# Performance work log

Hardware: AMD Instinct MI355X
Metric: run time of the kernel (lower is better)

## Reference

```python
import jax, jax.numpy as jnp
import numpy as np

N_NODES = 10000
N_EDGES = 320000
IN_DIM = 128
HID = 256


def setup_inputs() -> dict:
    key = jax.random.key(0)
    ks = jax.random.split(key, 10)
    s_in = 1.0 / np.sqrt(IN_DIM)
    s_h = 1.0 / np.sqrt(HID)
    return {
        "x": jax.random.normal(ks[0], (N_NODES, IN_DIM), dtype=jnp.float32),
        "edge_index": jax.random.randint(ks[1], (2, N_EDGES), 0, N_NODES, dtype=jnp.int64),
        # feature_projector Linear(IN_DIM -> HID)
        "Wp": jax.random.uniform(ks[2], (IN_DIM, HID), jnp.float32, -s_in, s_in),
        "bp": jax.random.uniform(ks[3], (HID,), jnp.float32, -s_in, s_in),
        # LSTM(input=HID, hidden=HID) params, torch layout [4H, H], gate order i,f,g,o
        "W_ih": jax.random.uniform(ks[4], (4 * HID, HID), jnp.float32, -s_h, s_h),
        "W_hh": jax.random.uniform(ks[5], (4 * HID, HID), jnp.float32, -s_h, s_h),
        "b_ih": jax.random.uniform(ks[6], (4 * HID,), jnp.float32, -s_h, s_h),
        "b_hh": jax.random.uniform(ks[7], (4 * HID,), jnp.float32, -s_h, s_h),
        # EvolveGCN-O initial weight [H, H] (glorot-style)
        "initial_weight": jax.random.normal(ks[8], (HID, HID), dtype=jnp.float32) * np.sqrt(2.0 / (2 * HID)),
        # GCNConv bias
        "b_gcn": jnp.zeros((HID,), dtype=jnp.float32),
    }


def _forward(x, edge_index, Wp, bp, W_ih, W_hh, b_ih, b_hh, initial_weight, b_gcn):
    n = x.shape[0]
    # 1) feature projection
    h = x @ Wp + bp  # [N, H]
    # 2) EvolveGCN-O: one LSTM step on the weight matrix (rows = batch),
    #    with h0 = c0 = initial_weight; evolved hidden state is the GCN weight.
    gates = initial_weight @ W_ih.T + b_ih + initial_weight @ W_hh.T + b_hh  # [H, 4H]
    i_g, f_g, g_g, o_g = jnp.split(gates, 4, axis=-1)
    c = jax.nn.sigmoid(f_g) * initial_weight + jax.nn.sigmoid(i_g) * jnp.tanh(g_g)
    W = jax.nn.sigmoid(o_g) * jnp.tanh(c)  # [H, H]
    # 3) GCN propagation with fixed W: out = D^{-1/2}(A+I)D^{-1/2} (h W) + b
    hw = h @ W  # [N, H]
    self_loop = jnp.arange(n, dtype=edge_index.dtype)
    src = jnp.concatenate([edge_index[0], self_loop])
    dst = jnp.concatenate([edge_index[1], self_loop])
    ones = jnp.ones(src.shape[0], dtype=hw.dtype)
    deg = jax.ops.segment_sum(ones, dst, num_segments=n)  # in-degree incl. self loop
    dinv = jnp.where(deg > 0, jax.lax.rsqrt(deg), 0.0)
    norm = dinv[src] * dinv[dst]  # [E+N]
    out = jax.ops.segment_sum(hw[src] * norm[:, None], dst, num_segments=n)
    return out + b_gcn


def reference(x, edge_index, Wp, bp, W_ih, W_hh, b_ih, b_hh, initial_weight, b_gcn):
    return _forward(x, edge_index, Wp, bp, W_ih, W_hh, b_ih, b_hh, initial_weight, b_gcn)
```

## Files before the change

kernel.cpp:

```cpp
#include <hip/hip_runtime.h>
#include <math.h>

#define N_NODES 10000
#define N_EDGES 320000
#define IN_DIM  128
#define HID     256
#define CAP     128
#define NWB     64
#define NFB     448
#define NXB     128
#define NB1     (NWB + NFB + NXB)

typedef __attribute__((ext_vector_type(8))) short frag_ab;
typedef __attribute__((ext_vector_type(4))) float frag_cd;


__device__ __forceinline__ unsigned bf16rne(float f) {
    union { float f; unsigned u; } c; c.f = f;
    return (c.u + 0x7FFFu + ((c.u >> 16) & 1u)) >> 16;
}
__device__ __forceinline__ float sig_f(float x)  { return 1.f / (1.f + __expf(-x)); }
__device__ __forceinline__ float tanh_f(float x) { return 1.f - 2.f / (1.f + __expf(2.f * x)); }

__global__ __launch_bounds__(256, 2)
void k1_prep(const float* __restrict__ x, const int* __restrict__ ei,
             const float* __restrict__ Wp, const float* __restrict__ bp,
             const float* __restrict__ wih, const float* __restrict__ whh,
             const float* __restrict__ b_ih, const float* __restrict__ b_hh,
             const float* __restrict__ iw,
             int* __restrict__ cursor, unsigned* __restrict__ wct,
             float* __restrict__ bc, unsigned* __restrict__ xb,
             int* __restrict__ bucket) {
    __shared__ __align__(16) char smem_raw[57920];
    const int bid = blockIdx.x;
    const int t = threadIdx.x;

    if (bid < NWB) {
        float (*aT)[260]  = (float(*)[260])smem_raw;
        float (*bSt)[20]  = (float(*)[20])(smem_raw + 33280);
        float (*iwc)[260] = (float(*)[260])(smem_raw + 53760);
        #pragma unroll
        for (int n = 0; n < 16; ++n) {
            int nrow = (n >> 2) * 256 + 4 * bid + (n & 3);
            bSt[t][n] = wih[nrow * 256 + t] + whh[nrow * 256 + t];
        }
        const int mg = t >> 2, ng = t & 3;
        const int srow = t >> 3, sf4 = t & 7;
        float acc[4][4] = {};
        for (int kt = 0; kt < 8; ++kt) {
            int k0 = kt * 32;
            __syncthreads();
            #pragma unroll
            for (int rr = 0; rr < 8; ++rr) {
                int row = srow + 32 * rr;
                float4 v = *(const float4*)&iw[row * 256 + k0 + 4 * sf4];
                aT[4 * sf4 + 0][row] = v.x; aT[4 * sf4 + 1][row] = v.y;
                aT[4 * sf4 + 2][row] = v.z; aT[4 * sf4 + 3][row] = v.w;
            }
            __syncthreads();
            if (kt == (bid >> 3)) {
                int c0 = (4 * bid) & 31;
                #pragma unroll
                for (int jj = 0; jj < 4; ++jj) iwc[jj][t] = aT[c0 + jj][t];
            }
            #pragma unroll 4
            for (int kk = 0; kk < 32; ++kk) {
                float4 a4 = *(const float4*)&aT[kk][4 * mg];
                float4 b4 = *(const float4*)&bSt[k0 + kk][4 * ng];
                float a[4] = {a4.x, a4.y, a4.z, a4.w};
                float b[4] = {b4.x, b4.y, b4.z, b4.w};
                #pragma unroll
                for (int i = 0; i < 4; ++i)
                    #pragma unroll
                    for (int j = 0; j < 4; ++j)
                        acc[i][j] = fmaf(a[i], b[j], acc[i][j]);
            }
        }
        float (*gates_lds)[17] = (float(*)[17])smem_raw;
        float (*wevc)[260]     = (float(*)[260])(smem_raw + 33280);
        __syncthreads();
        #pragma unroll
        for (int i = 0; i < 4; ++i)
            #pragma unroll
            for (int j = 0; j < 4; ++j)
                gates_lds[4 * mg + i][4 * ng + j] = acc[i][j];
        __syncthreads();
        {
            int r = t;
            #pragma unroll
            for (int jj = 0; jj < 4; ++jj) {
                int jcol = 4 * bid + jj;
                float gi = gates_lds[r][0  + jj] + b_ih[jcol]       + b_hh[jcol];
                float gf = gates_lds[r][4  + jj] + b_ih[256 + jcol] + b_hh[256 + jcol];
                float gg = gates_lds[r][8  + jj] + b_ih[512 + jcol] + b_hh[512 + jcol];
                float go = gates_lds[r][12 + jj] + b_ih[768 + jcol] + b_hh[768 + jcol];
                float c  = sig_f(gf) * iwc[jj][r] + sig_f(gi) * tanh_f(gg);
                wevc[jj][r] = sig_f(go) * tanh_f(c);
            }
        }
        float (*wpT)[132] = (float(*)[132])smem_raw;
        const int a2 = t & 63, jj = t >> 6;
        float c0 = 0.f, c1 = 0.f;
        for (int kt2 = 0; kt2 < 8; ++kt2) {
            int k0 = kt2 * 32;
            __syncthreads();
            #pragma unroll
            for (int ri = 0; ri < 4; ++ri) {
                int a = srow + 32 * ri;
                float4 v = *(const float4*)&Wp[a * 256 + k0 + 4 * sf4];
                wpT[4 * sf4 + 0][a] = v.x; wpT[4 * sf4 + 1][a] = v.y;
                wpT[4 * sf4 + 2][a] = v.z; wpT[4 * sf4 + 3][a] = v.w;
            }
            __syncthreads();
            #pragma unroll 8
            for (int kk = 0; kk < 32; ++kk) {
                float2 wv = *(const float2*)&wpT[kk][2 * a2];
                float wev = wevc[jj][k0 + kk];
                c0 = fmaf(wv.x, wev, c0);
                c1 = fmaf(wv.y, wev, c1);
            }
        }
        wct[(4 * bid + jj) * 64 + a2] = bf16rne(c0) | (bf16rne(c1) << 16);
        if (t < 4) {
            float s = 0.f;
            #pragma unroll 4
            for (int k4 = 0; k4 < 64; ++k4) {
                float4 b4 = *(const float4*)&bp[4 * k4];
                float4 w4 = *(const float4*)&wevc[t][4 * k4];
                s = fmaf(b4.x, w4.x, fmaf(b4.y, w4.y, fmaf(b4.z, w4.z, fmaf(b4.w, w4.w, s))));
            }
            bc[4 * bid + t] = s;
        }
    } else if (bid < NWB + NFB) {
        for (int u = (bid - NWB) * 256 + t; u < N_EDGES / 4; u += NFB * 256) {
            int4 s4 = *(const int4*)&ei[u * 4];
            int4 d4 = *(const int4*)&ei[N_EDGES + u * 4];
            int p0 = atomicAdd(&cursor[d4.x], 1);
            if (p0 < CAP) bucket[d4.x * CAP + p0] = s4.x;
            int p1 = atomicAdd(&cursor[d4.y], 1);
            if (p1 < CAP) bucket[d4.y * CAP + p1] = s4.y;
            int p2 = atomicAdd(&cursor[d4.z], 1);
            if (p2 < CAP) bucket[d4.z * CAP + p2] = s4.z;
            int p3 = atomicAdd(&cursor[d4.w], 1);
            if (p3 < CAP) bucket[d4.w * CAP + p3] = s4.w;
        }
    } else {
        const float4* x4 = (const float4*)x;
        uint2* xb2 = (uint2*)xb;
        for (int idx = (bid - NWB - NFB) * 256 + t; idx < N_NODES * 32; idx += NXB * 256) {
            float4 v = x4[idx];
            xb2[idx] = make_uint2(bf16rne(v.x) | (bf16rne(v.y) << 16),
                                  bf16rne(v.z) | (bf16rne(v.w) << 16));
        }
    }
}

__global__ __launch_bounds__(256)
void k2_agg_out(const unsigned* __restrict__ xb, const int* __restrict__ cursor,
                const int* __restrict__ bucket, const unsigned* __restrict__ wct,
                const float* __restrict__ bc, const float* __restrict__ b_gcn,
                float* __restrict__ out) {
    __shared__ unsigned y_lds[16][64];
    __shared__ float rs_lds[16];
    const int t = threadIdx.x;
    const int tile = blockIdx.x;
    const int w = t >> 6, lane = t & 63;
    const int q = lane >> 4, ln = lane & 15;

    for (int vi = 0; vi < 4; ++vi) {
        int r = vi * 4 + w;
        int v = tile * 16 + r;
        int cntv = cursor[v];
        float dv = rsqrtf((float)(cntv + 1));
        int cnt2 = cntv > CAP ? CAP : cntv;
        unsigned self = xb[v * 64 + lane];
        union { unsigned u; float f; } c0, c1;
        c0.u = self << 16; c1.u = self & 0xFFFF0000u;
        float acc0 = dv * c0.f, acc1 = dv * c1.f, wsum = dv;
        const int4* bkt4 = (const int4*)&bucket[v * CAP];
        int j = 0;
        for (; j + 8 <= cnt2; j += 8) {
            int4 sa = bkt4[j >> 2];
            int4 sb = bkt4[(j >> 2) + 1];
            float w0 = rsqrtf((float)(cursor[sa.x] + 1));
            float w1 = rsqrtf((float)(cursor[sa.y] + 1));
            float w2 = rsqrtf((float)(cursor[sa.z] + 1));
            float w3 = rsqrtf((float)(cursor[sa.w] + 1));
            float w4 = rsqrtf((float)(cursor[sb.x] + 1));
            float w5 = rsqrtf((float)(cursor[sb.y] + 1));
            float w6 = rsqrtf((float)(cursor[sb.z] + 1));
            float w7 = rsqrtf((float)(cursor[sb.w] + 1));
            unsigned r0 = xb[sa.x * 64 + lane];
            unsigned r1 = xb[sa.y * 64 + lane];
            unsigned r2 = xb[sa.z * 64 + lane];
            unsigned r3 = xb[sa.w * 64 + lane];
            unsigned r4 = xb[sb.x * 64 + lane];
            unsigned r5 = xb[sb.y * 64 + lane];
            unsigned r6 = xb[sb.z * 64 + lane];
            unsigned r7 = xb[sb.w * 64 + lane];
            union { unsigned u; float f; } a0, a1;
            a0.u = r0 << 16; a1.u = r0 & 0xFFFF0000u;
            acc0 = fmaf(w0, a0.f, acc0); acc1 = fmaf(w0, a1.f, acc1);
            a0.u = r1 << 16; a1.u = r1 & 0xFFFF0000u;
            acc0 = fmaf(w1, a0.f, acc0); acc1 = fmaf(w1, a1.f, acc1);
            a0.u = r2 << 16; a1.u = r2 & 0xFFFF0000u;
            acc0 = fmaf(w2, a0.f, acc0); acc1 = fmaf(w2, a1.f, acc1);
            a0.u = r3 << 16; a1.u = r3 & 0xFFFF0000u;
            acc0 = fmaf(w3, a0.f, acc0); acc1 = fmaf(w3, a1.f, acc1);
            a0.u = r4 << 16; a1.u = r4 & 0xFFFF0000u;
            acc0 = fmaf(w4, a0.f, acc0); acc1 = fmaf(w4, a1.f, acc1);
            a0.u = r5 << 16; a1.u = r5 & 0xFFFF0000u;
            acc0 = fmaf(w5, a0.f, acc0); acc1 = fmaf(w5, a1.f, acc1);
            a0.u = r6 << 16; a1.u = r6 & 0xFFFF0000u;
            acc0 = fmaf(w6, a0.f, acc0); acc1 = fmaf(w6, a1.f, acc1);
            a0.u = r7 << 16; a1.u = r7 & 0xFFFF0000u;
            acc0 = fmaf(w7, a0.f, acc0); acc1 = fmaf(w7, a1.f, acc1);
            wsum += w0 + w1 + w2 + w3 + w4 + w5 + w6 + w7;
        }
        for (; j < cnt2; ++j) {
            int s = bucket[v * CAP + j];
            float ws = rsqrtf((float)(cursor[s] + 1));
            unsigned rr = xb[s * 64 + lane];
            union { unsigned u; float f; } a0, a1;
            a0.u = rr << 16; a1.u = rr & 0xFFFF0000u;
            acc0 = fmaf(ws, a0.f, acc0); acc1 = fmaf(ws, a1.f, acc1);
            wsum += ws;
        }
        y_lds[r][lane] = bf16rne(dv * acc0) | (bf16rne(dv * acc1) << 16);
        if (lane == 0) rs_lds[r] = dv * wsum;
    }
    __syncthreads();

    const int4* ya   = (const int4*)&y_lds[0][0];
    const int4* wct4 = (const int4*)wct;
    union { int4 v; frag_ab f; } a[4];
    #pragma unroll
    for (int kc = 0; kc < 4; ++kc)
        a[kc].v = ya[ln * 16 + kc * 4 + q];
    float rsv[4];
    #pragma unroll
    for (int r = 0; r < 4; ++r) rsv[r] = rs_lds[q * 4 + r];
    #pragma unroll
    for (int i = 0; i < 4; ++i) {
        int n0 = (w + 4 * i) * 16;
        union { int4 v; frag_ab f; } b[4];
        #pragma unroll
        for (int kc = 0; kc < 4; ++kc)
            b[kc].v = wct4[(n0 + ln) * 16 + kc * 4 + q];
        frag_cd accd = {0.f, 0.f, 0.f, 0.f};
        #pragma unroll
        for (int kc = 0; kc < 4; ++kc)
            accd = __builtin_amdgcn_mfma_f32_16x16x32_bf16(a[kc].f, b[kc].f, accd, 0, 0, 0);
        int n = n0 + ln;
        float bcv = bc[n], bgv = b_gcn[n];
        #pragma unroll
        for (int r = 0; r < 4; ++r) {
            int m = tile * 16 + q * 4 + r;
            out[m * HID + n] = accd[r] + rsv[r] * bcv + bgv;
        }
    }
}

extern "C" void kernel_launch(void* const* d_in, const int* in_sizes, int n_in,
                              void* d_out, int out_size, void* d_ws, size_t ws_size,
                              hipStream_t stream) {
    const float* x     = (const float*)d_in[0];
    const int*   ei    = (const int*)d_in[1];
    const float* Wp    = (const float*)d_in[2];
    const float* bp    = (const float*)d_in[3];
    const float* W_ih  = (const float*)d_in[4];
    const float* W_hh  = (const float*)d_in[5];
    const float* b_ih  = (const float*)d_in[6];
    const float* b_hh  = (const float*)d_in[7];
    const float* iw    = (const float*)d_in[8];
    const float* b_gcn = (const float*)d_in[9];
    float* out = (float*)d_out;

    char* ws = (char*)d_ws;
    int*      cursor = (int*)     (ws + 0);
    unsigned* wct    = (unsigned*)(ws + 40064);
    float*    bc     = (float*)   (ws + 105600);
    unsigned* xb     = (unsigned*)(ws + 106624);
    int*      bucket = (int*)     (ws + 2666624);

    hipMemsetAsync(cursor, 0, N_NODES * sizeof(int), stream);

    k1_prep<<<NB1, 256, 0, stream>>>(x, ei, Wp, bp, W_ih, W_hh, b_ih, b_hh, iw,
                                     cursor, wct, bc, xb, bucket);
    k2_agg_out<<<625, 256, 0, stream>>>(xb, cursor, bucket, wct, bc, b_gcn, out);
}
```

Before: 150.4 us.

## Split fused prep and aggregate/output kernels into four separate kernels

Breaks the heterogeneous prep kernel into a weight-evolution kernel and a bucket/convert kernel, and splits aggregation from the MFMA output GEMM. Aggregation now uses one wave per node across 2500 blocks and writes the bf16 aggregate and row scale to a global workspace, which k_out reads back. This is meant to give the gather stage more parallelism and to stop the LSTM blocks from stalling the edge-bucketing blocks. In exchange it adds two kernel launches and a global round trip for the intermediate, and the weight kernel now runs alone with only 64 blocks, serialized before the bucketing kernel on the same stream.

```diff
diff --git a/kernel.cpp b/kernel.cpp
--- a/kernel.cpp
+++ b/kernel.cpp
@@ -7,9 +7,9 @@
 #define HID     256
 #define CAP     128
 #define NWB     64
+#define NXB     128
 #define NFB     448
-#define NXB     128
-#define NB1     (NWB + NFB + NXB)
+#define NBB     (NXB + NFB)
 
 typedef __attribute__((ext_vector_type(8))) short frag_ab;
 typedef __attribute__((ext_vector_type(4))) float frag_cd;
@@ -23,116 +23,128 @@
 __device__ __forceinline__ float tanh_f(float x) { return 1.f - 2.f / (1.f + __expf(2.f * x)); }
 
 __global__ __launch_bounds__(256, 2)
-void k1_prep(const float* __restrict__ x, const int* __restrict__ ei,
-             const float* __restrict__ Wp, const float* __restrict__ bp,
-             const float* __restrict__ wih, const float* __restrict__ whh,
-             const float* __restrict__ b_ih, const float* __restrict__ b_hh,
-             const float* __restrict__ iw,
-             int* __restrict__ cursor, unsigned* __restrict__ wct,
-             float* __restrict__ bc, unsigned* __restrict__ xb,
-             int* __restrict__ bucket) {
+void k_w(const float* __restrict__ Wp, const float* __restrict__ bp,
+         const float* __restrict__ wih, const float* __restrict__ whh,
+         const float* __restrict__ b_ih, const float* __restrict__ b_hh,
+         const float* __restrict__ iw,
+         unsigned* __restrict__ wct, float* __restrict__ bc) {
     __shared__ __align__(16) char smem_raw[57920];
     const int bid = blockIdx.x;
     const int t = threadIdx.x;
 
-    if (bid < NWB) {
-        float (*aT)[260]  = (float(*)[260])smem_raw;
-        float (*bSt)[20]  = (float(*)[20])(smem_raw + 33280);
-        float (*iwc)[260] = (float(*)[260])(smem_raw + 53760);
-        #pragma unroll
-        for (int n = 0; n < 16; ++n) {
-            int nrow = (n >> 2) * 256 + 4 * bid + (n & 3);
-            bSt[t][n] = wih[nrow * 256 + t] + whh[nrow * 256 + t];
-        }
-        const int mg = t >> 2, ng = t & 3;
-        const int srow = t >> 3, sf4 = t & 7;
-        float acc[4][4] = {};
-        for (int kt = 0; kt < 8; ++kt) {
-            int k0 = kt * 32;
-            __syncthreads();
+    float (*aT)[260]  = (float(*)[260])smem_raw;
+    float (*bSt)[20]  = (float(*)[20])(smem_raw + 33280);
+    float (*iwc)[260] = (float(*)[260])(smem_raw + 53760);
+    #pragma unroll
+    for (int n = 0; n < 16; ++n) {
+        int nrow = (n >> 2) * 256 + 4 * bid + (n & 3);
+        bSt[t][n] = wih[nrow * 256 + t] + whh[nrow * 256 + t];
+    }
+    const int mg = t >> 2, ng = t & 3;
+    const int srow = t >> 3, sf4 = t & 7;
+    float acc[4][4] = {};
+    for (int kt = 0; kt < 8; ++kt) {
+        int k0 = kt * 32;
+        __syncthreads();
+        #pragma unroll
+        for (int rr = 0; rr < 8; ++rr) {
+            int row = srow + 32 * rr;
+            float4 v = *(const float4*)&iw[row * 256 + k0 + 4 * sf4];
+            aT[4 * sf4 + 0][row] = v.x; aT[4 * sf4 + 1][row] = v.y;
+            aT[4 * sf4 + 2][row] = v.z; aT[4 * sf4 + 3][row] = v.w;
+        }
+        __syncthreads();
+        if (kt == (bid >> 3)) {
+            int c0 = (4 * bid) & 31;
             #pragma unroll
-            for (int rr = 0; rr < 8; ++rr) {
-                int row = srow + 32 * rr;
-                float4 v = *(const float4*)&iw[row * 256 + k0 + 4 * sf4];
-                aT[4 * sf4 + 0][row] = v.x; aT[4 * sf4 + 1][row] = v.y;
-                aT[4 * sf4 + 2][row] = v.z; aT[4 * sf4 + 3][row] = v.w;
-            }
-            __syncthreads();
-            if (kt == (bid >> 3)) {
-                int c0 = (4 * bid) & 31;
+            for (int jj = 0; jj < 4; ++jj) iwc[jj][t] = aT[c0 + jj][t];
+        }
+        #pragma unroll 4
+        for (int kk = 0; kk < 32; ++kk) {
+            float4 a4 = *(const float4*)&aT[kk][4 * mg];
+            float4 b4 = *(const float4*)&bSt[k0 + kk][4 * ng];
+            float a[4] = {a4.x, a4.y, a4.z, a4.w};
+            float b[4] = {b4.x, b4.y, b4.z, b4.w};
+            #pragma unroll
+            for (int i = 0; i < 4; ++i)
                 #pragma unroll
-                for (int jj = 0; jj < 4; ++jj) iwc[jj][t] = aT[c0 + jj][t];
-            }
-            #pragma unroll 4
-            for (int kk = 0; kk < 32; ++kk) {
-                float4 a4 = *(const float4*)&aT[kk][4 * mg];
-                float4 b4 = *(const float4*)&bSt[k0 + kk][4 * ng];
-                float a[4] = {a4.x, a4.y, a4.z, a4.w};
-                float b[4] = {b4.x, b4.y, b4.z, b4.w};
-                #pragma unroll
-                for (int i = 0; i < 4; ++i)
-                    #pragma unroll
-                    for (int j = 0; j < 4; ++j)
-                        acc[i][j] = fmaf(a[i], b[j], acc[i][j]);
-            }
-        }
-        float (*gates_lds)[17] = (float(*)[17])smem_raw;
-        float (*wevc)[260]     = (float(*)[260])(smem_raw + 33280);
-        __syncthreads();
-        #pragma unroll
-        for (int i = 0; i < 4; ++i)
-            #pragma unroll
-            for (int j = 0; j < 4; ++j)
-                gates_lds[4 * mg + i][4 * ng + j] = acc[i][j];
-        __syncthreads();
-        {
-            int r = t;
-            #pragma unroll
-            for (int jj = 0; jj < 4; ++jj) {
-                int jcol = 4 * bid + jj;
-                float gi = gates_lds[r][0  + jj] + b_ih[jcol]       + b_hh[jcol];
-                float gf = gates_lds[r][4  + jj] + b_ih[256 + jcol] + b_hh[256 + jcol];
-                float gg = gates_lds[r][8  + jj] + b_ih[512 + jcol] + b_hh[512 + jcol];
-                float go = gates_lds[r][12 + jj] + b_ih[768 + jcol] + b_hh[768 + jcol];
-                float c  = sig_f(gf) * iwc[jj][r] + sig_f(gi) * tanh_f(gg);
-                wevc[jj][r] = sig_f(go) * tanh_f(c);
-            }
-        }
-        float (*wpT)[132] = (float(*)[132])smem_raw;
-        const int a2 = t & 63, jj = t >> 6;
-        float c0 = 0.f, c1 = 0.f;
-        for (int kt2 = 0; kt2 < 8; ++kt2) {
-            int k0 = kt2 * 32;
-            __syncthreads();
-            #pragma unroll
-            for (int ri = 0; ri < 4; ++ri) {
-                int a = srow + 32 * ri;
-                float4 v = *(const float4*)&Wp[a * 256 + k0 + 4 * sf4];
-                wpT[4 * sf4 + 0][a] = v.x; wpT[4 * sf4 + 1][a] = v.y;
-                wpT[4 * sf4 + 2][a] = v.z; wpT[4 * sf4 + 3][a] = v.w;
-            }
-            __syncthreads();
-            #pragma unroll 8
-            for (int kk = 0; kk < 32; ++kk) {
-                float2 wv = *(const float2*)&wpT[kk][2 * a2];
-                float wev = wevc[jj][k0 + kk];
-                c0 = fmaf(wv.x, wev, c0);
-                c1 = fmaf(wv.y, wev, c1);
-            }
-        }
-        wct[(4 * bid + jj) * 64 + a2] = bf16rne(c0) | (bf16rne(c1) << 16);
-        if (t < 4) {
-            float s = 0.f;
-            #pragma unroll 4
-            for (int k4 = 0; k4 < 64; ++k4) {
-                float4 b4 = *(const float4*)&bp[4 * k4];
-                float4 w4 = *(const float4*)&wevc[t][4 * k4];
-                s = fmaf(b4.x, w4.x, fmaf(b4.y, w4.y, fmaf(b4.z, w4.z, fmaf(b4.w, w4.w, s))));
-            }
-            bc[4 * bid + t] = s;
-        }
-    } else if (bid < NWB + NFB) {
-        for (int u = (bid - NWB) * 256 + t; u < N_EDGES / 4; u += NFB * 256) {
+                for (int j = 0; j < 4; ++j)
+                    acc[i][j] = fmaf(a[i], b[j], acc[i][j]);
+        }
+    }
+    float (*gates_lds)[17] = (float(*)[17])smem_raw;
+    float (*wevc)[260]     = (float(*)[260])(smem_raw + 33280);
+    __syncthreads();
+    #pragma unroll
+    for (int i = 0; i < 4; ++i)
+        #pragma unroll
+        for (int j = 0; j < 4; ++j)
+            gates_lds[4 * mg + i][4 * ng + j] = acc[i][j];
+    __syncthreads();
+    {
+        int r = t;
+        #pragma unroll
+        for (int jj = 0; jj < 4; ++jj) {
+            int jcol = 4 * bid + jj;
+            float gi = gates_lds[r][0  + jj] + b_ih[jcol]       + b_hh[jcol];
+            float gf = gates_lds[r][4  + jj] + b_ih[256 + jcol] + b_hh[256 + jcol];
+            float gg = gates_lds[r][8  + jj] + b_ih[512 + jcol] + b_hh[512 + jcol];
+            float go = gates_lds[r][12 + jj] + b_ih[768 + jcol] + b_hh[768 + jcol];
+            float c  = sig_f(gf) * iwc[jj][r] + sig_f(gi) * tanh_f(gg);
+            wevc[jj][r] = sig_f(go) * tanh_f(c);
+        }
+    }
+    float (*wpT)[132] = (float(*)[132])smem_raw;
+    const int a2 = t & 63, jj = t >> 6;
+    float c0 = 0.f, c1 = 0.f;
+    for (int kt2 = 0; kt2 < 8; ++kt2) {
+        int k0 = kt2 * 32;
+        __syncthreads();
+        #pragma unroll
+        for (int ri = 0; ri < 4; ++ri) {
+            int a = srow + 32 * ri;
+            float4 v = *(const float4*)&Wp[a * 256 + k0 + 4 * sf4];
+            wpT[4 * sf4 + 0][a] = v.x; wpT[4 * sf4 + 1][a] = v.y;
+            wpT[4 * sf4 + 2][a] = v.z; wpT[4 * sf4 + 3][a] = v.w;
+        }
+        __syncthreads();
+        #pragma unroll 8
+        for (int kk = 0; kk < 32; ++kk) {
+            float2 wv = *(const float2*)&wpT[kk][2 * a2];
+            float wev = wevc[jj][k0 + kk];
+            c0 = fmaf(wv.x, wev, c0);
+            c1 = fmaf(wv.y, wev, c1);
+        }
+    }
+    wct[(4 * bid + jj) * 64 + a2] = bf16rne(c0) | (bf16rne(c1) << 16);
+    if (t < 4) {
+        float s = 0.f;
+        #pragma unroll 4
+        for (int k4 = 0; k4 < 64; ++k4) {
+            float4 b4 = *(const float4*)&bp[4 * k4];
+            float4 w4 = *(const float4*)&wevc[t][4 * k4];
+            s = fmaf(b4.x, w4.x, fmaf(b4.y, w4.y, fmaf(b4.z, w4.z, fmaf(b4.w, w4.w, s))));
+        }
+        bc[4 * bid + t] = s;
+    }
+}
+
+__global__ __launch_bounds__(256)
+void k_b(const float* __restrict__ x, const int* __restrict__ ei,
+         int* __restrict__ cursor, unsigned* __restrict__ xb,
+         int* __restrict__ bucket) {
+    const int bid = blockIdx.x;
+    const int t = threadIdx.x;
+    if (bid < NXB) {
+        const float4* x4 = (const float4*)x;
+        uint2* xb2 = (uint2*)xb;
+        for (int idx = bid * 256 + t; idx < N_NODES * 32; idx += NXB * 256) {
+            float4 v = x4[idx];
+            xb2[idx] = make_uint2(bf16rne(v.x) | (bf16rne(v.y) << 16),
+                                  bf16rne(v.z) | (bf16rne(v.w) << 16));
+        }
+    } else {
+        for (int u = (bid - NXB) * 256 + t; u < N_EDGES / 4; u += NFB * 256) {
             int4 s4 = *(const int4*)&ei[u * 4];
             int4 d4 = *(const int4*)&ei[N_EDGES + u * 4];
             int p0 = atomicAdd(&cursor[d4.x], 1);
@@ -144,102 +156,92 @@
             int p3 = atomicAdd(&cursor[d4.w], 1);
             if (p3 < CAP) bucket[d4.w * CAP + p3] = s4.w;
         }
-    } else {
-        const float4* x4 = (const float4*)x;
-        uint2* xb2 = (uint2*)xb;
-        for (int idx = (bid - NWB - NFB) * 256 + t; idx < N_NODES * 32; idx += NXB * 256) {
-            float4 v = x4[idx];
-            xb2[idx] = make_uint2(bf16rne(v.x) | (bf16rne(v.y) << 16),
-                                  bf16rne(v.z) | (bf16rne(v.w) << 16));
-        }
     }
 }
 
 __global__ __launch_bounds__(256)
-void k2_agg_out(const unsigned* __restrict__ xb, const int* __restrict__ cursor,
-                const int* __restrict__ bucket, const unsigned* __restrict__ wct,
-                const float* __restrict__ bc, const float* __restrict__ b_gcn,
-                float* __restrict__ out) {
-    __shared__ unsigned y_lds[16][64];
-    __shared__ float rs_lds[16];
+void k_agg(const unsigned* __restrict__ xb, const int* __restrict__ cursor,
+           const int* __restrict__ bucket, unsigned* __restrict__ yb,
+           float* __restrict__ rs) {
     const int t = threadIdx.x;
-    const int tile = blockIdx.x;
-    const int w = t >> 6, lane = t & 63;
-    const int q = lane >> 4, ln = lane & 15;
-
-    for (int vi = 0; vi < 4; ++vi) {
-        int r = vi * 4 + w;
-        int v = tile * 16 + r;
-        int cntv = cursor[v];
-        float dv = rsqrtf((float)(cntv + 1));
-        int cnt2 = cntv > CAP ? CAP : cntv;
-        unsigned self = xb[v * 64 + lane];
-        union { unsigned u; float f; } c0, c1;
-        c0.u = self << 16; c1.u = self & 0xFFFF0000u;
-        float acc0 = dv * c0.f, acc1 = dv * c1.f, wsum = dv;
-        const int4* bkt4 = (const int4*)&bucket[v * CAP];
-        int j = 0;
-        for (; j + 8 <= cnt2; j += 8) {
-            int4 sa = bkt4[j >> 2];
-            int4 sb = bkt4[(j >> 2) + 1];
-            float w0 = rsqrtf((float)(cursor[sa.x] + 1));
-            float w1 = rsqrtf((float)(cursor[sa.y] + 1));
-            float w2 = rsqrtf((float)(cursor[sa.z] + 1));
-            float w3 = rsqrtf((float)(cursor[sa.w] + 1));
-            float w4 = rsqrtf((float)(cursor[sb.x] + 1));
-            float w5 = rsqrtf((float)(cursor[sb.y] + 1));
-            float w6 = rsqrtf((float)(cursor[sb.z] + 1));
-            float w7 = rsqrtf((float)(cursor[sb.w] + 1));
-            unsigned r0 = xb[sa.x * 64 + lane];
-            unsigned r1 = xb[sa.y * 64 + lane];
-            unsigned r2 = xb[sa.z * 64 + lane];
-            unsigned r3 = xb[sa.w * 64 + lane];
-            unsigned r4 = xb[sb.x * 64 + lane];
-            unsigned r5 = xb[sb.y * 64 + lane];
-            unsigned r6 = xb[sb.z * 64 + lane];
-            unsigned r7 = xb[sb.w * 64 + lane];
-            union { unsigned u; float f; } a0, a1;
-            a0.u = r0 << 16; a1.u = r0 & 0xFFFF0000u;
-            acc0 = fmaf(w0, a0.f, acc0); acc1 = fmaf(w0, a1.f, acc1);
-            a0.u = r1 << 16; a1.u = r1 & 0xFFFF0000u;
-            acc0 = fmaf(w1, a0.f, acc0); acc1 = fmaf(w1, a1.f, acc1);
-            a0.u = r2 << 16; a1.u = r2 & 0xFFFF0000u;
-            acc0 = fmaf(w2, a0.f, acc0); acc1 = fmaf(w2, a1.f, acc1);
-            a0.u = r3 << 16; a1.u = r3 & 0xFFFF0000u;
-            acc0 = fmaf(w3, a0.f, acc0); acc1 = fmaf(w3, a1.f, acc1);
-            a0.u = r4 << 16; a1.u = r4 & 0xFFFF0000u;
-            acc0 = fmaf(w4, a0.f, acc0); acc1 = fmaf(w4, a1.f, acc1);
-            a0.u = r5 << 16; a1.u = r5 & 0xFFFF0000u;
-            acc0 = fmaf(w5, a0.f, acc0); acc1 = fmaf(w5, a1.f, acc1);
-            a0.u = r6 << 16; a1.u = r6 & 0xFFFF0000u;
-            acc0 = fmaf(w6, a0.f, acc0); acc1 = fmaf(w6, a1.f, acc1);
-            a0.u = r7 << 16; a1.u = r7 & 0xFFFF0000u;
-            acc0 = fmaf(w7, a0.f, acc0); acc1 = fmaf(w7, a1.f, acc1);
-            wsum += w0 + w1 + w2 + w3 + w4 + w5 + w6 + w7;
-        }
-        for (; j < cnt2; ++j) {
-            int s = bucket[v * CAP + j];
-            float ws = rsqrtf((float)(cursor[s] + 1));
-            unsigned rr = xb[s * 64 + lane];
-            union { unsigned u; float f; } a0, a1;
-            a0.u = rr << 16; a1.u = rr & 0xFFFF0000u;
-            acc0 = fmaf(ws, a0.f, acc0); acc1 = fmaf(ws, a1.f, acc1);
-            wsum += ws;
-        }
-        y_lds[r][lane] = bf16rne(dv * acc0) | (bf16rne(dv * acc1) << 16);
-        if (lane == 0) rs_lds[r] = dv * wsum;
-    }
-    __syncthreads();
-
-    const int4* ya   = (const int4*)&y_lds[0][0];
+    const int wv = t >> 6, lane = t & 63;
+    const int v = blockIdx.x * 4 + wv;
+    int cntv = cursor[v];
+    float dv = rsqrtf((float)(cntv + 1));
+    int cnt2 = cntv > CAP ? CAP : cntv;
+    unsigned self = xb[v * 64 + lane];
+    union { unsigned u; float f; } c0, c1;
+    c0.u = self << 16; c1.u = self & 0xFFFF0000u;
+    float acc0 = dv * c0.f, acc1 = dv * c1.f, wsum = dv;
+    const int4* bkt4 = (const int4*)&bucket[v * CAP];
+    int j = 0;
+    for (; j + 8 <= cnt2; j += 8) {
+        int4 sa = bkt4[j >> 2];
+        int4 sb = bkt4[(j >> 2) + 1];
+        float w0 = rsqrtf((float)(cursor[sa.x] + 1));
+        float w1 = rsqrtf((float)(cursor[sa.y] + 1));
+        float w2 = rsqrtf((float)(cursor[sa.z] + 1));
+        float w3 = rsqrtf((float)(cursor[sa.w] + 1));
+        float w4 = rsqrtf((float)(cursor[sb.x] + 1));
+        float w5 = rsqrtf((float)(cursor[sb.y] + 1));
+        float w6 = rsqrtf((float)(cursor[sb.z] + 1));
+        float w7 = rsqrtf((float)(cursor[sb.w] + 1));
+        unsigned r0 = xb[sa.x * 64 + lane];
+        unsigned r1 = xb[sa.y * 64 + lane];
+        unsigned r2 = xb[sa.z * 64 + lane];
+        unsigned r3 = xb[sa.w * 64 + lane];
+        unsigned r4 = xb[sb.x * 64 + lane];
+        unsigned r5 = xb[sb.y * 64 + lane];
+        unsigned r6 = xb[sb.z * 64 + lane];
+        unsigned r7 = xb[sb.w * 64 + lane];
+        union { unsigned u; float f; } a0, a1;
+        a0.u = r0 << 16; a1.u = r0 & 0xFFFF0000u;
+        acc0 = fmaf(w0, a0.f, acc0); acc1 = fmaf(w0, a1.f, acc1);
+        a0.u = r1 << 16; a1.u = r1 & 0xFFFF0000u;
+        acc0 = fmaf(w1, a0.f, acc0); acc1 = fmaf(w1, a1.f, acc1);
+        a0.u = r2 << 16; a1.u = r2 & 0xFFFF0000u;
+        acc0 = fmaf(w2, a0.f, acc0); acc1 = fmaf(w2, a1.f, acc1);
+        a0.u = r3 << 16; a1.u = r3 & 0xFFFF0000u;
+        acc0 = fmaf(w3, a0.f, acc0); acc1 = fmaf(w3, a1.f, acc1);
+        a0.u = r4 << 16; a1.u = r4 & 0xFFFF0000u;
+        acc0 = fmaf(w4, a0.f, acc0); acc1 = fmaf(w4, a1.f, acc1);
+        a0.u = r5 << 16; a1.u = r5 & 0xFFFF0000u;
+        acc0 = fmaf(w5, a0.f, acc0); acc1 = fmaf(w5, a1.f, acc1);
+        a0.u = r6 << 16; a1.u = r6 & 0xFFFF0000u;
+        acc0 = fmaf(w6, a0.f, acc0); acc1 = fmaf(w6, a1.f, acc1);
+        a0.u = r7 << 16; a1.u = r7 & 0xFFFF0000u;
+        acc0 = fmaf(w7, a0.f, acc0); acc1 = fmaf(w7, a1.f, acc1);
+        wsum += w0 + w1 + w2 + w3 + w4 + w5 + w6 + w7;
+    }
+    for (; j < cnt2; ++j) {
+        int s = bucket[v * CAP + j];
+        float ws = rsqrtf((float)(cursor[s] + 1));
+        unsigned rr = xb[s * 64 + lane];
+        union { unsigned u; float f; } a0, a1;
+        a0.u = rr << 16; a1.u = rr & 0xFFFF0000u;
+        acc0 = fmaf(ws, a0.f, acc0); acc1 = fmaf(ws, a1.f, acc1);
+        wsum += ws;
+    }
+    yb[v * 64 + lane] = bf16rne(dv * acc0) | (bf16rne(dv * acc1) << 16);
+    if (lane == 0) rs[v] = dv * wsum;
+}
+
+__global__ __launch_bounds__(256)
+void k_out(const unsigned* __restrict__ yb, const unsigned* __restrict__ wct,
+           const float* __restrict__ bc, const float* __restrict__ rs,
+           const float* __restrict__ b_gcn, float* __restrict__ out) {
+    int m0 = blockIdx.x * 16;
+    int w = threadIdx.x >> 6, lane = threadIdx.x & 63;
+    int q = lane >> 4, ln = lane & 15;
+    const int4* yb4  = (const int4*)yb;
     const int4* wct4 = (const int4*)wct;
     union { int4 v; frag_ab f; } a[4];
     #pragma unroll
     for (int kc = 0; kc < 4; ++kc)
-        a[kc].v = ya[ln * 16 + kc * 4 + q];
+        a[kc].v = yb4[(m0 + ln) * 16 + kc * 4 + q];
     float rsv[4];
     #pragma unroll
-    for (int r = 0; r < 4; ++r) rsv[r] = rs_lds[q * 4 + r];
+    for (int r = 0; r < 4; ++r) rsv[r] = rs[m0 + q * 4 + r];
     #pragma unroll
     for (int i = 0; i < 4; ++i) {
         int n0 = (w + 4 * i) * 16;
@@ -247,16 +249,16 @@
         #pragma unroll
         for (int kc = 0; kc < 4; ++kc)
             b[kc].v = wct4[(n0 + ln) * 16 + kc * 4 + q];
-        frag_cd accd = {0.f, 0.f, 0.f, 0.f};
+        frag_cd acc = {0.f, 0.f, 0.f, 0.f};
         #pragma unroll
         for (int kc = 0; kc < 4; ++kc)
-            accd = __builtin_amdgcn_mfma_f32_16x16x32_bf16(a[kc].f, b[kc].f, accd, 0, 0, 0);
+            acc = __builtin_amdgcn_mfma_f32_16x16x32_bf16(a[kc].f, b[kc].f, acc, 0, 0, 0);
         int n = n0 + ln;
         float bcv = bc[n], bgv = b_gcn[n];
         #pragma unroll
         for (int r = 0; r < 4; ++r) {
-            int m = tile * 16 + q * 4 + r;
-            out[m * HID + n] = accd[r] + rsv[r] * bcv + bgv;
+            int m = m0 + q * 4 + r;
+            out[m * HID + n] = acc[r] + rsv[r] * bcv + bgv;
         }
     }
 }
@@ -281,11 +283,14 @@
     unsigned* wct    = (unsigned*)(ws + 40064);
     float*    bc     = (float*)   (ws + 105600);
     unsigned* xb     = (unsigned*)(ws + 106624);
-    int*      bucket = (int*)     (ws + 2666624);
+    unsigned* yb     = (unsigned*)(ws + 2666624);
+    float*    rs     = (float*)   (ws + 5226624);
+    int*      bucket = (int*)     (ws + 5266624);
 
     hipMemsetAsync(cursor, 0, N_NODES * sizeof(int), stream);
 
-    k1_prep<<<NB1, 256, 0, stream>>>(x, ei, Wp, bp, W_ih, W_hh, b_ih, b_hh, iw,
-                                     cursor, wct, bc, xb, bucket);
-    k2_agg_out<<<625, 256, 0, stream>>>(xb, cursor, bucket, wct, bc, b_gcn, out);
-}
+    k_w  <<<NWB, 256, 0, stream>>>(Wp, bp, W_ih, W_hh, b_ih, b_hh, iw, wct, bc);
+    k_b  <<<NBB, 256, 0, stream>>>(x, ei, cursor, xb, bucket);
+    k_agg<<<2500, 256, 0, stream>>>(xb, cursor, bucket, yb, rs);
+    k_out<<<625, 256, 0, stream>>>(yb, wct, bc, rs, b_gcn, out);
+}
```

Measured after the change: 155.7 us. +3.5%, slower.
